# Kernel optimization log

Measured on AMD Instinct MI355X. Metric: run time of the kernel, lower is better.

The kernel has to match this reference:

```python
import jax, jax.numpy as jnp
import numpy as np

LSTM_SIZE = 512
MEM_SIZE = 2048
MEM_DIM = 256
NB_READS = 4
GAMMA = 0.95
EPS = 1e-8
B = 64
IN_RAW = 256
IN_TOTAL = IN_RAW + NB_READS * MEM_SIZE  # 8448
PARAM_DIM = (2 * MEM_DIM + 1) * NB_READS  # 2052


def setup_inputs() -> dict:
    key = jax.random.key(0)
    ks = jax.random.split(key, 8)
    s = 0.02
    return {
        "x": jax.random.normal(ks[0], (B, IN_RAW), jnp.float32),
        "M": jax.random.normal(ks[1], (B, MEM_SIZE, MEM_DIM), jnp.float32),
        "wu": jax.random.uniform(ks[2], (B, MEM_SIZE), jnp.float32),
        "wr": jax.random.uniform(ks[3], (B, NB_READS * MEM_SIZE), jnp.float32),
        "h0": jnp.zeros((LSTM_SIZE,), jnp.float32),
        "c0": jnp.zeros((LSTM_SIZE,), jnp.float32),
        "W_ih": jax.random.normal(ks[4], (4 * LSTM_SIZE, IN_TOTAL), jnp.float32) * s,
        "W_hh": jax.random.normal(ks[5], (4 * LSTM_SIZE, LSTM_SIZE), jnp.float32) * s,
        "b_ih": jnp.zeros((4 * LSTM_SIZE,), jnp.float32),
        "b_hh": jnp.zeros((4 * LSTM_SIZE,), jnp.float32),
        "W_p": jax.random.normal(ks[6], (PARAM_DIM, LSTM_SIZE), jnp.float32) * s,
        "b_p": jax.random.uniform(ks[7], (PARAM_DIM,), jnp.float32, -0.1, 0.1),
    }


def _lstm_scan(x_seq, h0, c0, W_ih, W_hh, b):
    # torch treats the 2-D input as an unbatched sequence of length B:
    # the recurrence runs across the batch axis with a single shared state.
    xW = x_seq @ W_ih.T + b  # [B, 4H] precomputed input contribution

    def step(carry, xw):
        h, c = carry
        g = xw + h @ W_hh.T
        i, f, gg, o = jnp.split(g, 4)
        c = jax.nn.sigmoid(f) * c + jax.nn.sigmoid(i) * jnp.tanh(gg)
        h = jax.nn.sigmoid(o) * jnp.tanh(c)
        return (h, c), h

    (hf, cf), hs = jax.lax.scan(step, (h0, c0), xW)
    return hs, hf, cf


def reference(x, M, wu, wr, h0, c0, W_ih, W_hh, b_ih, b_hh, W_p, b_p):
    ctrl_in = jnp.concatenate([x, wr], axis=-1)  # [B, IN_TOTAL]
    hs, hf, cf = _lstm_scan(ctrl_in, h0, c0, W_ih, W_hh, b_ih + b_hh)
    param = hs @ W_p.T + b_p  # [B, PARAM_DIM]

    nd = NB_READS * MEM_DIM
    k = jnp.tanh(param[:, :nd]).reshape(B, NB_READS, MEM_DIM)
    a = jnp.tanh(param[:, nd:2 * nd]).reshape(B, NB_READS, MEM_DIM)
    sig_alpha = jax.nn.sigmoid(param[:, -NB_READS:])  # [B, R]

    # least_used: topk(wu, k=MEM_SIZE) == full descending sort of indices
    order = jnp.argsort(-wu, axis=-1)  # [B, MEM_SIZE]
    lu_idx = order[:, -1]  # least used slot
    wlu = jax.nn.one_hot(order[:, -NB_READS:], MEM_SIZE, dtype=M.dtype).sum(1)  # [B, N]

    # read head addressing: cosine similarity softmax
    ip = jnp.einsum('brd,bnd->brn', k, M)  # [B, R, N]
    k_norm = jnp.sqrt(jnp.sum(k * k, -1))[:, :, None]
    M_norm = jnp.sqrt(jnp.sum(M * M, -1))[:, None, :]
    wr_t = jax.nn.softmax(ip / (k_norm * M_norm + EPS), axis=-1)  # [B, R, N]

    # write head addressing
    wr_prev3 = wr.reshape(B, NB_READS, MEM_SIZE)
    sa = sig_alpha[:, :, None]
    ww_t = sa * wr_prev3 + (1.0 - sa) * wlu[:, None, :]  # [B, R, N]

    wu_t = GAMMA * wu + wr_t.sum(1) + ww_t.sum(1)  # [B, N]

    erase = 1.0 - jax.nn.one_hot(lu_idx, MEM_SIZE, dtype=M.dtype)  # [B, N]
    M_t = M * erase[:, :, None] + jnp.einsum('brn,brd->bnd', ww_t, a)  # [B, N, D]
    r_t = jnp.einsum('brn,bnd->brd', wr_t, M_t).reshape(B, nd)  # [B, R*D]

    return jnp.concatenate([hs, r_t], axis=-1)  # [B, LSTM+R*D]
```

## Files before the change

kernel.cpp:

```cpp
#include <hip/hip_runtime.h>
#include <hip/hip_bf16.h>

#define BB 64
#define IN_RAW_ 256
#define KIN_ 8448
#define WRW 8192
#define PD_ 2052
#define XW_KS 11
#define XW_CH 768

__global__ __launch_bounds__(256) void k_xw_partial(
    const float* __restrict__ x, const float* __restrict__ wr,
    const float* __restrict__ Wih, float* __restrict__ xwp) {
  const int jb = blockIdx.x & 31;
  const int ks = blockIdx.x >> 5;
  const int j0 = jb << 6;
  const int k0 = ks * XW_CH;
  __shared__ __align__(16) float As[32][68];
  __shared__ __align__(16) float Bs[32][68];
  const int tid = threadIdx.x;
  const int ti = tid & 15, tj = tid >> 4;
  const int lt = tid >> 2, lq = tid & 3;
  float acc[4][4];
#pragma unroll
  for (int i = 0; i < 4; ++i)
#pragma unroll
    for (int j = 0; j < 4; ++j) acc[i][j] = 0.f;
  for (int kc = 0; kc < XW_CH; kc += 32) {
    __syncthreads();
    const int kb = k0 + kc + (lq << 3);
    float va[8], vb[8];
    if (kb < IN_RAW_) {
      const float* p = x + lt * IN_RAW_ + kb;
#pragma unroll
      for (int u = 0; u < 8; ++u) va[u] = p[u];
    } else {
      const float* p = wr + (size_t)lt * WRW + (kb - IN_RAW_);
#pragma unroll
      for (int u = 0; u < 8; ++u) va[u] = p[u];
    }
    {
      const float* p = Wih + (size_t)(j0 + lt) * KIN_ + kb;
#pragma unroll
      for (int u = 0; u < 8; ++u) vb[u] = p[u];
    }
#pragma unroll
    for (int u = 0; u < 8; ++u) As[(lq << 3) + u][lt] = va[u];
#pragma unroll
    for (int u = 0; u < 8; ++u) Bs[(lq << 3) + u][lt] = vb[u];
    __syncthreads();
#pragma unroll
    for (int kk = 0; kk < 32; ++kk) {
      const float4 a4 = *(const float4*)&As[kk][ti << 2];
      const float4 b4 = *(const float4*)&Bs[kk][tj << 2];
      const float av[4] = {a4.x, a4.y, a4.z, a4.w};
      const float bv[4] = {b4.x, b4.y, b4.z, b4.w};
#pragma unroll
      for (int i = 0; i < 4; ++i)
#pragma unroll
        for (int j = 0; j < 4; ++j) acc[i][j] = fmaf(av[i], bv[j], acc[i][j]);
    }
  }
#pragma unroll
  for (int i = 0; i < 4; ++i) {
    const int t = (ti << 2) + i;
    float* dst = xwp + ((size_t)(ks * BB + t) << 11) + j0 + (tj << 2);
    dst[0] = acc[i][0]; dst[1] = acc[i][1]; dst[2] = acc[i][2]; dst[3] = acc[i][3];
  }
}

__global__ __launch_bounds__(64, 1) void k_scan(
    const float* __restrict__ xwp, const float* __restrict__ bih,
    const float* __restrict__ bhh, const float* __restrict__ Whh,
    const float* __restrict__ h0, const float* __restrict__ c0,
    unsigned long long* __restrict__ ht, unsigned long long* __restrict__ xwt,
    float* __restrict__ out, const float* __restrict__ wu,
    int* __restrict__ t4) {
  const int W = blockIdx.x;
  const int l = threadIdx.x;
  if (W >= 192) {
    const int t = W - 192;
    for (int i = 0; i < 32; ++i) {
      const int col = (i << 6) + l;
      float s = bih[col] + bhh[col];
#pragma unroll
      for (int ks = 0; ks < XW_KS; ++ks)
        s += xwp[(size_t)ks * 131072 + (t << 11) + col];
      const unsigned long long pk =
          (1ull << 32) | (unsigned long long)__float_as_uint(s);
      __hip_atomic_store(xwt + (t << 11) + col, pk, __ATOMIC_RELAXED,
                         __HIP_MEMORY_SCOPE_AGENT);
    }
    return;
  }
  if (W >= 128) {
    const int b = W - 128;
    float val[32];
#pragma unroll
    for (int i = 0; i < 32; ++i) val[i] = wu[(b << 11) + (i << 6) + l];
    for (int pick = 0; pick < 4; ++pick) {
      float bv = 3.4e38f; int bi = -1;
// ... 1 lines not shown
      for (int i = 0; i < 32; ++i) {
        const int n = (i << 6) + l;
        const float v = val[i];
        if (v < bv || (v == bv && n > bi)) { bv = v; bi = n; }
      }
#pragma unroll
      for (int s = 1; s < 64; s <<= 1) {
        const float ov = __shfl_xor(bv, s);
        const int oi = __shfl_xor(bi, s);
        if (ov < bv || (ov == bv && oi > bi)) { bv = ov; bi = oi; }
      }
      if (l == 0) t4[(b << 2) + pick] = bi;
      if ((bi & 63) == l) val[bi >> 6] = 3.4e38f;
    }
    return;
  }
  const int d = l & 3;
  const int jj = (W << 2) + d;
  float wreg[16][8];
#pragma unroll
  for (int r = 0; r < 16; ++r) {
    const int row = ((r >> 2) << 9) + (W << 2) + (r & 3);
    const float* p = Whh + ((size_t)row << 9) + (l << 3);
#pragma unroll
    for (int u = 0; u < 8; ++u) wreg[r][u] = p[u];
  }
  float c = 0.f;
  if (l < 4) c = c0[jj];
  float h[8];
#pragma unroll
  for (int u = 0; u < 8; ++u) h[u] = h0[(l << 3) + u];

  for (int t = 0; t < 64; ++t) {
    float xv0 = 0, xv1 = 0, xv2 = 0, xv3 = 0;
    if (l < 4) {
      const unsigned long long* xp = xwt + (t << 11) + jj;
      unsigned long long x0, x1, x2, x3;
      for (;;) {
        x0 = __hip_atomic_load(xp, __ATOMIC_RELAXED, __HIP_MEMORY_SCOPE_AGENT);
        x1 = __hip_atomic_load(xp + 512, __ATOMIC_RELAXED, __HIP_MEMORY_SCOPE_AGENT);
        x2 = __hip_atomic_load(xp + 1024, __ATOMIC_RELAXED, __HIP_MEMORY_SCOPE_AGENT);
        x3 = __hip_atomic_load(xp + 1536, __ATOMIC_RELAXED, __HIP_MEMORY_SCOPE_AGENT);
        if ((unsigned)((x0 & x1 & x2 & x3) >> 32) == 1u) break;
      }
      xv0 = __uint_as_float((unsigned)x0);
      xv1 = __uint_as_float((unsigned)x1);
      xv2 = __uint_as_float((unsigned)x2);
      xv3 = __uint_as_float((unsigned)x3);
    }
    if (t > 0) {
      const unsigned long long* hp = ht + (t << 9) + (l << 3);
      unsigned long long va[8], vb[8];
#pragma unroll
      for (int u = 0; u < 8; ++u)
        va[u] = __hip_atomic_load(hp + u, __ATOMIC_RELAXED, __HIP_MEMORY_SCOPE_AGENT);
      for (;;) {
#pragma unroll
        for (int u = 0; u < 8; ++u)
          vb[u] = __hip_atomic_load(hp + u, __ATOMIC_RELAXED, __HIP_MEMORY_SCOPE_AGENT);
        bool ra = true;
#pragma unroll
        for (int u = 0; u < 8; ++u) ra &= ((unsigned)(va[u] >> 32) == (unsigned)t);
        if (ra) break;
#pragma unroll
        for (int u = 0; u < 8; ++u)
          va[u] = __hip_atomic_load(hp + u, __ATOMIC_RELAXED, __HIP_MEMORY_SCOPE_AGENT);
        bool rb_ = true;
#pragma unroll
        for (int u = 0; u < 8; ++u) rb_ &= ((unsigned)(vb[u] >> 32) == (unsigned)t);
        if (rb_) {
#pragma unroll
          for (int u = 0; u < 8; ++u) va[u] = vb[u];
          break;
        }
      }
#pragma unroll
      for (int u = 0; u < 8; ++u) h[u] = __uint_as_float((unsigned)va[u]);
    }
    float pr[16];
#pragma unroll
    for (int r = 0; r < 16; ++r) {
      float s = 0.f;
#pragma unroll
      for (int u = 0; u < 8; ++u) s = fmaf(wreg[r][u], h[u], s);
      pr[r] = s;
    }
    float v8[8], v4[4], v2[2], v1;
    {
      const bool b0 = (l & 1) != 0;
#pragma unroll
      for (int j = 0; j < 8; ++j) {
        const float keep = b0 ? pr[2 * j + 1] : pr[2 * j];
        const float send = b0 ? pr[2 * j] : pr[2 * j + 1];
        v8[j] = keep + __shfl_xor(send, 1);
      }
    }
    {
      const bool b1 = (l & 2) != 0;
#pragma unroll
      for (int j = 0; j < 4; ++j) {
        const float keep = b1 ? v8[2 * j + 1] : v8[2 * j];
        const float send = b1 ? v8[2 * j] : v8[2 * j + 1];
        v4[j] = keep + __shfl_xor(send, 2);
      }
    }
    {
      const bool b2 = (l & 4) != 0;
#pragma unroll
      for (int j = 0; j < 2; ++j) {
        const float keep = b2 ? v4[2 * j + 1] : v4[2 * j];
// ... 71 lines not shown
#pragma unroll
    for (int u = 0; u < 8; ++u) As[(lq << 3) + u][lt] = va[u];
#pragma unroll
    for (int u = 0; u < 8; ++u) Bs[(lq << 3) + u][lt] = vb[u];
    __syncthreads();
#pragma unroll
    for (int kk = 0; kk < 32; ++kk) {
      const float4 a4 = *(const float4*)&As[kk][ti << 2];
      const float4 b4 = *(const float4*)&Bs[kk][tj << 2];
      const float av[4] = {a4.x, a4.y, a4.z, a4.w};
      const float bv[4] = {b4.x, b4.y, b4.z, b4.w};
#pragma unroll
      for (int i = 0; i < 4; ++i)
#pragma unroll
        for (int j = 0; j < 4; ++j) acc[i][j] = fmaf(av[i], bv[j], acc[i][j]);
    }
  }
#pragma unroll
  for (int i = 0; i < 4; ++i) {
    const int b = (ti << 2) + i;
#pragma unroll
    for (int j = 0; j < 4; ++j) {
      const int col = j0 + (tj << 2) + j;
      if (col < PD_) {
        const float v = acc[i][j] + bp[col];
        if (col < 1024) km[(b << 10) + col] = tanhf(v);
        else if (col < 2048) am[(b << 10) + col - 1024] = tanhf(v);
        else sa[(b << 2) + col - 2048] = 1.f / (1.f + expf(-v));
      }
    }
  }
}

__global__ __launch_bounds__(256) void k_ip(
    const float* __restrict__ M, const float* __restrict__ km,
    float* __restrict__ ip, float* __restrict__ mn) {
  const int b = blockIdx.x >> 4;
  const int nb = blockIdx.x & 15;
  const int n0 = nb << 7;
  const int tid = threadIdx.x;
  const int wv = tid >> 6, l = tid & 63;
  const int q = l >> 4, l16 = l & 15;
  float kr[4][16];
#pragma unroll
  for (int r = 0; r < 4; ++r)
#pragma unroll
    for (int cc = 0; cc < 4; ++cc) {
      const float4 kv = *(const float4*)(km + (((b << 2) + r) << 8) + (cc << 6) + (l16 << 2));
      kr[r][(cc << 2) + 0] = kv.x; kr[r][(cc << 2) + 1] = kv.y;
      kr[r][(cc << 2) + 2] = kv.z; kr[r][(cc << 2) + 3] = kv.w;
    }
  for (int it = 0; it < 8; ++it) {
    const int n = n0 + (wv << 5) + (it << 2) + q;
    const float* mrow = M + (((size_t)b << 11) + n) * 256;
    float s[4] = {0.f, 0.f, 0.f, 0.f};
    float sm = 0.f;
#pragma unroll
    for (int cc = 0; cc < 4; ++cc) {
      const float4 m4 = *(const float4*)(mrow + (cc << 6) + (l16 << 2));
      const float mv[4] = {m4.x, m4.y, m4.z, m4.w};
#pragma unroll
      for (int e = 0; e < 4; ++e) {
        sm = fmaf(mv[e], mv[e], sm);
#pragma unroll
        for (int r = 0; r < 4; ++r) s[r] = fmaf(kr[r][(cc << 2) + e], mv[e], s[r]);
      }
    }
#pragma unroll
    for (int r = 0; r < 4; ++r) {
      float v = s[r];
      v += __shfl_xor(v, 1); v += __shfl_xor(v, 2); v += __shfl_xor(v, 4); v += __shfl_xor(v, 8);
      s[r] = v;
    }
    sm += __shfl_xor(sm, 1); sm += __shfl_xor(sm, 2); sm += __shfl_xor(sm, 4); sm += __shfl_xor(sm, 8);
    if (l16 == 0) {
      const size_t base = ((size_t)b) << 13;
      ip[base + n] = s[0];
      ip[base + 2048 + n] = s[1];
      ip[base + 4096 + n] = s[2];
      ip[base + 6144 + n] = s[3];
      mn[(b << 11) + n] = sqrtf(sm);
    }
  }
}

__global__ __launch_bounds__(512) void k_smrt(
    const float* __restrict__ ip, const float* __restrict__ mn_g,
    const float* __restrict__ sa_g, const float* __restrict__ wr_in,
    const int* __restrict__ t4, const float* __restrict__ am,
    const float* __restrict__ M, const float* __restrict__ km,
    float* __restrict__ out) {
  const int b = blockIdx.x;
  const int tid = threadIdx.x;
  const int wv = tid >> 6, l = tid & 63;
  __shared__ float lam[4][2048];
  __shared__ float mnl[2048];
  __shared__ float Sd[16];
  __shared__ float t4s[4];
  __shared__ float Sl[16];
  __shared__ float wlu4[4];
#pragma unroll
  for (int i = 0; i < 4; ++i) mnl[tid + (i << 9)] = mn_g[(b << 11) + tid + (i << 9)];
  __syncthreads();
  if (wv < 4) {
    const int r = wv;
    const float* kp = km + (b << 10) + (r << 8);
    float sq = 0.f;
#pragma unroll
    for (int i = 0; i < 4; ++i) { const float v = kp[l + (i << 6)]; sq = fmaf(v, v, sq); }
    sq += __shfl_xor(sq, 1);  sq += __shfl_xor(sq, 2);  sq += __shfl_xor(sq, 4);
    sq += __shfl_xor(sq, 8);  sq += __shfl_xor(sq, 16); sq += __shfl_xor(sq, 32);
    const float kn = sqrtf(sq);
    const float* ipr = ip + (((size_t)b) << 13) + ((size_t)r << 11);
    float mx = -3.4e38f;
#pragma unroll 4
    for (int i = 0; i < 32; ++i) {
      const int n = l + (i << 6);
      const float v = ipr[n] / fmaf(kn, mnl[n], 1e-8f);
      lam[r][n] = v;
      mx = fmaxf(mx, v);
    }
    mx = fmaxf(mx, __shfl_xor(mx, 1));  mx = fmaxf(mx, __shfl_xor(mx, 2));
    mx = fmaxf(mx, __shfl_xor(mx, 4));  mx = fmaxf(mx, __shfl_xor(mx, 8));
    mx = fmaxf(mx, __shfl_xor(mx, 16)); mx = fmaxf(mx, __shfl_xor(mx, 32));
    float sum = 0.f;
#pragma unroll 4
    for (int i = 0; i < 32; ++i) {
      const int n = l + (i << 6);
      const float e = expf(lam[r][n] - mx);
      lam[r][n] = e;
      sum += e;
    }
    sum += __shfl_xor(sum, 1);  sum += __shfl_xor(sum, 2);  sum += __shfl_xor(sum, 4);
    sum += __shfl_xor(sum, 8);  sum += __shfl_xor(sum, 16); sum += __shfl_xor(sum, 32);
    const float inv = 1.f / sum;
#pragma unroll 4
    for (int i = 0; i < 32; ++i) {
      const int n = l + (i << 6);
      lam[r][n] *= inv;
    }
  }
  __syncthreads();
#pragma unroll
  for (int j = 0; j < 2; ++j) {
    const int pr = (wv << 1) + j;
    const int r = pr >> 2, qq = pr & 3;
    const float* wp = wr_in + (size_t)b * WRW + (qq << 11);
    float s = 0.f;
#pragma unroll 4
    for (int i = 0; i < 32; ++i) {
      const int n = l + (i << 6);
      s = fmaf(lam[r][n], wp[n], s);
    }
    s += __shfl_xor(s, 1);  s += __shfl_xor(s, 2);  s += __shfl_xor(s, 4);
    s += __shfl_xor(s, 8);  s += __shfl_xor(s, 16); s += __shfl_xor(s, 32);
    if (l == 0) Sd[pr] = s;
  }
  if (tid < 4) {
    float s = 0.f;
#pragma unroll
    for (int ii = 0; ii < 4; ++ii) s += lam[tid][t4[(b << 2) + ii]];
    t4s[tid] = s;
    wlu4[tid] = lam[tid][t4[b << 2]];
  }
  __syncthreads();
  if (tid < 16) {
    const int r = tid >> 2, qq = tid & 3;
    const float sv = sa_g[(b << 2) + qq];
    Sl[tid] = sv * Sd[tid] + (1.f - sv) * t4s[r];
  }
  __syncthreads();
  float4 acc[4];
#pragma unroll
  for (int r = 0; r < 4; ++r) acc[r] = make_float4(0.f, 0.f, 0.f, 0.f);
  const float* Mb = M + (((size_t)b << 11)) * 256;
#pragma unroll 4
  for (int it = 0; it < 256; ++it) {
    const int n = (wv << 8) + it;
    const float4 m4 = *(const float4*)(Mb + (size_t)n * 256 + (l << 2));
#pragma unroll
    for (int r = 0; r < 4; ++r) {
      const float w_ = lam[r][n];
      acc[r].x = fmaf(w_, m4.x, acc[r].x);
      acc[r].y = fmaf(w_, m4.y, acc[r].y);
      acc[r].z = fmaf(w_, m4.z, acc[r].z);
      acc[r].w = fmaf(w_, m4.w, acc[r].w);
    }
  }
  __syncthreads();
  float* red = &lam[0][0];
#pragma unroll
  for (int r = 0; r < 4; ++r)
    *(float4*)(red + (((wv << 2) + r) << 8) + (l << 2)) = acc[r];
  __syncthreads();
  const int luv = t4[b << 2];
#pragma unroll
  for (int i = 0; i < 2; ++i) {
    const int e = tid + (i << 9);
    const int r = e >> 8, d = e & 255;
    float s = -wlu4[r] * M[(((size_t)b << 11) + luv) * 256 + d];
#pragma unroll
    for (int qq = 0; qq < 4; ++qq)
      s = fmaf(Sl[(r << 2) + qq], am[(((b << 2) + qq) << 8) + d], s);
#pragma unroll
    for (int w2 = 0; w2 < 8; ++w2)
      s += red[(((w2 << 2) + r) << 8) + d];
    out[b * 1536 + 512 + e] = s;
  }
}

extern "C" void kernel_launch(void* const* d_in, const int* in_sizes, int n_in,
                              void* d_out, int out_size, void* d_ws, size_t ws_size,
                              hipStream_t stream) {
  (void)in_sizes; (void)n_in; (void)out_size;
  const float* x   = (const float*)d_in[0];
  const float* M   = (const float*)d_in[1];
  const float* wu  = (const float*)d_in[2];
  const float* wr  = (const float*)d_in[3];
  const float* h0  = (const float*)d_in[4];
  const float* c0  = (const float*)d_in[5];
  const float* Wih = (const float*)d_in[6];
  const float* Whh = (const float*)d_in[7];
  const float* bih = (const float*)d_in[8];
  const float* bhh = (const float*)d_in[9];
  const float* Wp  = (const float*)d_in[10];
  const float* bp  = (const float*)d_in[11];
  float* out = (float*)d_out;
  char* ws = (char*)d_ws;
  if (ws_size < 10229760u) return;

  float* xwp = (float*)(ws + 0);
  float* km  = (float*)(ws + 5767168);
  float* am  = (float*)(ws + 6029312);
  float* sa  = (float*)(ws + 6291456);
  int*   t4  = (int*)(ws + 6292480);
  float* ipb = (float*)(ws + 6293504);
  float* mnb = (float*)(ws + 8390656);
  unsigned long long* ht  = (unsigned long long*)(ws + 8914944);
  unsigned long long* xwt = (unsigned long long*)(ws + 9181184);

  hipMemsetAsync(ws + 8914944, 0, 266240 + 1048576, stream);
  hipLaunchKernelGGL(k_xw_partial, dim3(352), dim3(256), 0, stream, x, wr, Wih, xwp);
  hipLaunchKernelGGL(k_scan, dim3(256), dim3(64), 0, stream,
                     xwp, bih, bhh, Whh, h0, c0, ht, xwt, out, wu, t4);
  hipLaunchKernelGGL(k_param, dim3(33), dim3(256), 0, stream, out, Wp, bp, km, am, sa);
  hipLaunchKernelGGL(k_ip, dim3(1024), dim3(256), 0, stream, M, km, ipb, mnb);
  hipLaunchKernelGGL(k_smrt, dim3(64), dim3(512), 0, stream,
                     ipb, mnb, sa, wr, t4, am, M, km, out);
}
```

Measured before the change: 274.0 us.

## Replace tiled input GEMM with transposed-ctrl streaming kernel and reorder scan polling

The shared-memory tiled GEMM for the LSTM input projection is replaced by two kernels. The first transposes the concatenated controller input into a [K,64] layout. The second has each wave compute 8 output columns for all 64 timesteps, reading W_ih directly with per-lane coalesced activation loads and no LDS. In the scan kernel, the xW loads are issued before waiting on h, and the h-poll checks two sentinel words before fetching the remaining six. This trades an extra launch and transpose pass for more parallel blocks and lower-latency polling; the W_ih reads are now scalar and uncoalesced across lanes, which may hurt bandwidth.

```diff
diff --git a/kernel.cpp b/kernel.cpp
--- a/kernel.cpp
+++ b/kernel.cpp
@@ -7,66 +7,62 @@
 #define WRW 8192
 #define PD_ 2052
 #define XW_KS 11
-#define XW_CH 768
-
-__global__ __launch_bounds__(256) void k_xw_partial(
+
+__global__ __launch_bounds__(256) void k_ctrlT(
     const float* __restrict__ x, const float* __restrict__ wr,
-    const float* __restrict__ Wih, float* __restrict__ xwp) {
-  const int jb = blockIdx.x & 31;
-  const int ks = blockIdx.x >> 5;
-  const int j0 = jb << 6;
-  const int k0 = ks * XW_CH;
-  __shared__ __align__(16) float As[32][68];
-  __shared__ __align__(16) float Bs[32][68];
+    float* __restrict__ ctrlT) {
+  const int kb = blockIdx.x << 5;
   const int tid = threadIdx.x;
-  const int ti = tid & 15, tj = tid >> 4;
-  const int lt = tid >> 2, lq = tid & 3;
-  float acc[4][4];
-#pragma unroll
-  for (int i = 0; i < 4; ++i)
-#pragma unroll
-    for (int j = 0; j < 4; ++j) acc[i][j] = 0.f;
-  for (int kc = 0; kc < XW_CH; kc += 32) {
-    __syncthreads();
-    const int kb = k0 + kc + (lq << 3);
-    float va[8], vb[8];
-    if (kb < IN_RAW_) {
-      const float* p = x + lt * IN_RAW_ + kb;
-#pragma unroll
-      for (int u = 0; u < 8; ++u) va[u] = p[u];
-    } else {
-      const float* p = wr + (size_t)lt * WRW + (kb - IN_RAW_);
-#pragma unroll
-      for (int u = 0; u < 8; ++u) va[u] = p[u];
-    }
-    {
-      const float* p = Wih + (size_t)(j0 + lt) * KIN_ + kb;
-#pragma unroll
-      for (int u = 0; u < 8; ++u) vb[u] = p[u];
-    }
-#pragma unroll
-    for (int u = 0; u < 8; ++u) As[(lq << 3) + u][lt] = va[u];
-#pragma unroll
-    for (int u = 0; u < 8; ++u) Bs[(lq << 3) + u][lt] = vb[u];
-    __syncthreads();
-#pragma unroll
-    for (int kk = 0; kk < 32; ++kk) {
-      const float4 a4 = *(const float4*)&As[kk][ti << 2];
-      const float4 b4 = *(const float4*)&Bs[kk][tj << 2];
-      const float av[4] = {a4.x, a4.y, a4.z, a4.w};
-      const float bv[4] = {b4.x, b4.y, b4.z, b4.w};
-#pragma unroll
-      for (int i = 0; i < 4; ++i)
-#pragma unroll
-        for (int j = 0; j < 4; ++j) acc[i][j] = fmaf(av[i], bv[j], acc[i][j]);
-    }
-  }
-#pragma unroll
-  for (int i = 0; i < 4; ++i) {
-    const int t = (ti << 2) + i;
-    float* dst = xwp + ((size_t)(ks * BB + t) << 11) + j0 + (tj << 2);
-    dst[0] = acc[i][0]; dst[1] = acc[i][1]; dst[2] = acc[i][2]; dst[3] = acc[i][3];
-  }
+  __shared__ float ld[32][65];
+#pragma unroll
+  for (int pass = 0; pass < 8; ++pass) {
+    const int t = (tid >> 5) + (pass << 3);
+    const int k = tid & 31;
+    const int kk = kb + k;
+    const float v = (kk < IN_RAW_) ? x[t * IN_RAW_ + kk]
+                                   : wr[(size_t)t * WRW + kk - IN_RAW_];
+    ld[k][t] = v;
+  }
+  __syncthreads();
+#pragma unroll
+  for (int pass = 0; pass < 8; ++pass) {
+    const int k = (tid >> 6) + (pass << 2);
+    ctrlT[(size_t)(kb + k) * 64 + (tid & 63)] = ld[k][tid & 63];
+  }
+}
+
+__global__ __launch_bounds__(256) void k_xw2(
+    const float* __restrict__ ctrlT, const float* __restrict__ Wih,
+    float* __restrict__ xwp) {
+  const int cb = blockIdx.x & 63;
+  const int ks = blockIdx.x >> 6;
+  const int k0 = ks * 768;
+  const int wv = __builtin_amdgcn_readfirstlane(threadIdx.x >> 6);
+  const int l = threadIdx.x & 63;
+  const int c0 = (cb << 5) + (wv << 3);
+  const float* at = ctrlT + (size_t)k0 * 64 + l;
+  const float* wb = Wih + (size_t)c0 * KIN_ + k0;
+  float acc[8];
+#pragma unroll
+  for (int c = 0; c < 8; ++c) acc[c] = 0.f;
+#pragma unroll 2
+  for (int k = 0; k < 768; k += 4) {
+    const float a0 = at[(size_t)(k + 0) << 6];
+    const float a1 = at[(size_t)(k + 1) << 6];
+    const float a2 = at[(size_t)(k + 2) << 6];
+    const float a3 = at[(size_t)(k + 3) << 6];
+#pragma unroll
+    for (int c = 0; c < 8; ++c) {
+      const float* wp = wb + (size_t)c * KIN_ + k;
+      acc[c] = fmaf(a0, wp[0], acc[c]);
+      acc[c] = fmaf(a1, wp[1], acc[c]);
+      acc[c] = fmaf(a2, wp[2], acc[c]);
+      acc[c] = fmaf(a3, wp[3], acc[c]);
+    }
+  }
+  float* dst = xwp + (size_t)ks * 131072 + (l << 11) + c0;
+  *(float4*)(dst) = make_float4(acc[0], acc[1], acc[2], acc[3]);
+  *(float4*)(dst + 4) = make_float4(acc[4], acc[5], acc[6], acc[7]);
 }
 
 __global__ __launch_bounds__(64, 1) void k_scan(
@@ -134,50 +130,57 @@
   for (int u = 0; u < 8; ++u) h[u] = h0[(l << 3) + u];
 
   for (int t = 0; t < 64; ++t) {
+    const unsigned long long* xp = xwt + (t << 11) + jj;
+    unsigned long long x0 = 0, x1 = 0, x2 = 0, x3 = 0;
+    if (l < 4) {
+      x0 = __hip_atomic_load(xp, __ATOMIC_RELAXED, __HIP_MEMORY_SCOPE_AGENT);
+      x1 = __hip_atomic_load(xp + 512, __ATOMIC_RELAXED, __HIP_MEMORY_SCOPE_AGENT);
+      x2 = __hip_atomic_load(xp + 1024, __ATOMIC_RELAXED, __HIP_MEMORY_SCOPE_AGENT);
+      x3 = __hip_atomic_load(xp + 1536, __ATOMIC_RELAXED, __HIP_MEMORY_SCOPE_AGENT);
+    }
+    if (t > 0) {
+      const unsigned long long* hp = ht + (t << 9) + (l << 3);
+      unsigned long long v[8];
+      for (;;) {
+        const unsigned long long s0 =
+            __hip_atomic_load(hp, __ATOMIC_RELAXED, __HIP_MEMORY_SCOPE_AGENT);
+        const unsigned long long s4 =
+            __hip_atomic_load(hp + 4, __ATOMIC_RELAXED, __HIP_MEMORY_SCOPE_AGENT);
+        if (((unsigned)(s0 >> 32) == (unsigned)t) &&
+            ((unsigned)(s4 >> 32) == (unsigned)t)) {
+          v[0] = s0; v[4] = s4;
+          v[1] = __hip_atomic_load(hp + 1, __ATOMIC_RELAXED, __HIP_MEMORY_SCOPE_AGENT);
+          v[2] = __hip_atomic_load(hp + 2, __ATOMIC_RELAXED, __HIP_MEMORY_SCOPE_AGENT);
+          v[3] = __hip_atomic_load(hp + 3, __ATOMIC_RELAXED, __HIP_MEMORY_SCOPE_AGENT);
+          v[5] = __hip_atomic_load(hp + 5, __ATOMIC_RELAXED, __HIP_MEMORY_SCOPE_AGENT);
+          v[6] = __hip_atomic_load(hp + 6, __ATOMIC_RELAXED, __HIP_MEMORY_SCOPE_AGENT);
+          v[7] = __hip_atomic_load(hp + 7, __ATOMIC_RELAXED, __HIP_MEMORY_SCOPE_AGENT);
+          bool ok = true;
+          ok &= ((unsigned)(v[1] >> 32) == (unsigned)t);
+          ok &= ((unsigned)(v[2] >> 32) == (unsigned)t);
+          ok &= ((unsigned)(v[3] >> 32) == (unsigned)t);
+          ok &= ((unsigned)(v[5] >> 32) == (unsigned)t);
+          ok &= ((unsigned)(v[6] >> 32) == (unsigned)t);
+          ok &= ((unsigned)(v[7] >> 32) == (unsigned)t);
+          if (ok) break;
+        }
+      }
+#pragma unroll
+      for (int u = 0; u < 8; ++u) h[u] = __uint_as_float((unsigned)v[u]);
+    }
     float xv0 = 0, xv1 = 0, xv2 = 0, xv3 = 0;
     if (l < 4) {
-      const unsigned long long* xp = xwt + (t << 11) + jj;
-      unsigned long long x0, x1, x2, x3;
-      for (;;) {
+      while (!(((unsigned)(x0 >> 32) == 1u) && ((unsigned)(x1 >> 32) == 1u) &&
+               ((unsigned)(x2 >> 32) == 1u) && ((unsigned)(x3 >> 32) == 1u))) {
         x0 = __hip_atomic_load(xp, __ATOMIC_RELAXED, __HIP_MEMORY_SCOPE_AGENT);
         x1 = __hip_atomic_load(xp + 512, __ATOMIC_RELAXED, __HIP_MEMORY_SCOPE_AGENT);
         x2 = __hip_atomic_load(xp + 1024, __ATOMIC_RELAXED, __HIP_MEMORY_SCOPE_AGENT);
         x3 = __hip_atomic_load(xp + 1536, __ATOMIC_RELAXED, __HIP_MEMORY_SCOPE_AGENT);
-        if ((unsigned)((x0 & x1 & x2 & x3) >> 32) == 1u) break;
       }
       xv0 = __uint_as_float((unsigned)x0);
       xv1 = __uint_as_float((unsigned)x1);
       xv2 = __uint_as_float((unsigned)x2);
       xv3 = __uint_as_float((unsigned)x3);
-    }
-    if (t > 0) {
-      const unsigned long long* hp = ht + (t << 9) + (l << 3);
-      unsigned long long va[8], vb[8];
-#pragma unroll
-      for (int u = 0; u < 8; ++u)
-        va[u] = __hip_atomic_load(hp + u, __ATOMIC_RELAXED, __HIP_MEMORY_SCOPE_AGENT);
-      for (;;) {
-#pragma unroll
-        for (int u = 0; u < 8; ++u)
-          vb[u] = __hip_atomic_load(hp + u, __ATOMIC_RELAXED, __HIP_MEMORY_SCOPE_AGENT);
-        bool ra = true;
-#pragma unroll
-        for (int u = 0; u < 8; ++u) ra &= ((unsigned)(va[u] >> 32) == (unsigned)t);
-        if (ra) break;
-#pragma unroll
-        for (int u = 0; u < 8; ++u)
-          va[u] = __hip_atomic_load(hp + u, __ATOMIC_RELAXED, __HIP_MEMORY_SCOPE_AGENT);
-        bool rb_ = true;
-#pragma unroll
-        for (int u = 0; u < 8; ++u) rb_ &= ((unsigned)(vb[u] >> 32) == (unsigned)t);
-        if (rb_) {
-#pragma unroll
-          for (int u = 0; u < 8; ++u) va[u] = vb[u];
-          break;
-        }
-      }
-#pragma unroll
-      for (int u = 0; u < 8; ++u) h[u] = __uint_as_float((unsigned)va[u]);
     }
     float pr[16];
 #pragma unroll
@@ -510,7 +513,7 @@
   const float* bp  = (const float*)d_in[11];
   float* out = (float*)d_out;
   char* ws = (char*)d_ws;
-  if (ws_size < 10229760u) return;
+  if (ws_size < 12392448u) return;
 
   float* xwp = (float*)(ws + 0);
   float* km  = (float*)(ws + 5767168);
@@ -521,9 +524,11 @@
   float* mnb = (float*)(ws + 8390656);
   unsigned long long* ht  = (unsigned long long*)(ws + 8914944);
   unsigned long long* xwt = (unsigned long long*)(ws + 9181184);
+  float* ctrlT = (float*)(ws + 10229760);
 
   hipMemsetAsync(ws + 8914944, 0, 266240 + 1048576, stream);
-  hipLaunchKernelGGL(k_xw_partial, dim3(352), dim3(256), 0, stream, x, wr, Wih, xwp);
+  hipLaunchKernelGGL(k_ctrlT, dim3(264), dim3(256), 0, stream, x, wr, ctrlT);
+  hipLaunchKernelGGL(k_xw2, dim3(704), dim3(256), 0, stream, ctrlT, Wih, xwp);
   hipLaunchKernelGGL(k_scan, dim3(256), dim3(64), 0, stream,
                      xwp, bih, bhh, Whh, h0, c0, ht, xwt, out, wu, t4);
   hipLaunchKernelGGL(k_param, dim3(33), dim3(256), 0, stream, out, Wp, bp, km, am, sa);
```

After: 405.7 us. +48.0%, slower.

## Widen xW GEMM tiles to 64x128 with 16 K-splits and streamline scan polling

Applied to the files above, without the earlier changes.

The input-projection GEMM now uses 128-column tiles with 4x8 register accumulators and 16 K-slices of 544 (the last is 288), launching 256 blocks instead of 352. Each block reuses its A tile across twice as many columns and writes results as float4. The scan's spin-wait is restructured: xW loads are issued before the h wait, and h polling checks two sentinel words before loading the rest. The partial-sum buffer grows, which shifts workspace offsets, and the scan's reduction over K-slices must match the new XW_KS of 16.

```diff
diff --git a/kernel.cpp b/kernel.cpp
--- a/kernel.cpp
+++ b/kernel.cpp
@@ -6,30 +6,30 @@
 #define KIN_ 8448
 #define WRW 8192
 #define PD_ 2052
-#define XW_KS 11
-#define XW_CH 768
+#define XW_KS 16
 
 __global__ __launch_bounds__(256) void k_xw_partial(
     const float* __restrict__ x, const float* __restrict__ wr,
     const float* __restrict__ Wih, float* __restrict__ xwp) {
-  const int jb = blockIdx.x & 31;
-  const int ks = blockIdx.x >> 5;
-  const int j0 = jb << 6;
-  const int k0 = ks * XW_CH;
+  const int cb = blockIdx.x & 15;
+  const int ks = blockIdx.x >> 4;
+  const int j0 = cb << 7;
+  const int k0 = ks * 544;
+  const int klen = (ks == 15) ? 288 : 544;
   __shared__ __align__(16) float As[32][68];
-  __shared__ __align__(16) float Bs[32][68];
+  __shared__ __align__(16) float Bs[32][136];
   const int tid = threadIdx.x;
   const int ti = tid & 15, tj = tid >> 4;
   const int lt = tid >> 2, lq = tid & 3;
-  float acc[4][4];
+  float acc[4][8];
 #pragma unroll
   for (int i = 0; i < 4; ++i)
 #pragma unroll
-    for (int j = 0; j < 4; ++j) acc[i][j] = 0.f;
-  for (int kc = 0; kc < XW_CH; kc += 32) {
+    for (int j = 0; j < 8; ++j) acc[i][j] = 0.f;
+  for (int kc = 0; kc < klen; kc += 32) {
     __syncthreads();
     const int kb = k0 + kc + (lq << 3);
-    float va[8], vb[8];
+    float va[8], vb0[8], vb1[8];
     if (kb < IN_RAW_) {
       const float* p = x + lt * IN_RAW_ + kb;
 #pragma unroll
@@ -42,30 +42,38 @@
     {
       const float* p = Wih + (size_t)(j0 + lt) * KIN_ + kb;
 #pragma unroll
-      for (int u = 0; u < 8; ++u) vb[u] = p[u];
+      for (int u = 0; u < 8; ++u) vb0[u] = p[u];
+      const float* p2 = Wih + (size_t)(j0 + 64 + lt) * KIN_ + kb;
+#pragma unroll
+      for (int u = 0; u < 8; ++u) vb1[u] = p2[u];
     }
 #pragma unroll
     for (int u = 0; u < 8; ++u) As[(lq << 3) + u][lt] = va[u];
 #pragma unroll
-    for (int u = 0; u < 8; ++u) Bs[(lq << 3) + u][lt] = vb[u];
+    for (int u = 0; u < 8; ++u) Bs[(lq << 3) + u][lt] = vb0[u];
+#pragma unroll
+    for (int u = 0; u < 8; ++u) Bs[(lq << 3) + u][64 + lt] = vb1[u];
     __syncthreads();
 #pragma unroll
     for (int kk = 0; kk < 32; ++kk) {
       const float4 a4 = *(const float4*)&As[kk][ti << 2];
-      const float4 b4 = *(const float4*)&Bs[kk][tj << 2];
+      const float4 b4a = *(const float4*)&Bs[kk][tj << 3];
+      const float4 b4b = *(const float4*)&Bs[kk][(tj << 3) + 4];
       const float av[4] = {a4.x, a4.y, a4.z, a4.w};
-      const float bv[4] = {b4.x, b4.y, b4.z, b4.w};
+      const float bv[8] = {b4a.x, b4a.y, b4a.z, b4a.w,
+                           b4b.x, b4b.y, b4b.z, b4b.w};
 #pragma unroll
       for (int i = 0; i < 4; ++i)
 #pragma unroll
-        for (int j = 0; j < 4; ++j) acc[i][j] = fmaf(av[i], bv[j], acc[i][j]);
+        for (int j = 0; j < 8; ++j) acc[i][j] = fmaf(av[i], bv[j], acc[i][j]);
     }
   }
 #pragma unroll
   for (int i = 0; i < 4; ++i) {
     const int t = (ti << 2) + i;
-    float* dst = xwp + ((size_t)(ks * BB + t) << 11) + j0 + (tj << 2);
-    dst[0] = acc[i][0]; dst[1] = acc[i][1]; dst[2] = acc[i][2]; dst[3] = acc[i][3];
+    float* dst = xwp + (size_t)ks * 131072 + (t << 11) + j0 + (tj << 3);
+    *(float4*)(dst) = make_float4(acc[i][0], acc[i][1], acc[i][2], acc[i][3]);
+    *(float4*)(dst + 4) = make_float4(acc[i][4], acc[i][5], acc[i][6], acc[i][7]);
   }
 }
 
@@ -134,50 +142,57 @@
   for (int u = 0; u < 8; ++u) h[u] = h0[(l << 3) + u];
 
   for (int t = 0; t < 64; ++t) {
+    const unsigned long long* xp = xwt + (t << 11) + jj;
+    unsigned long long x0 = 0, x1 = 0, x2 = 0, x3 = 0;
+    if (l < 4) {
+      x0 = __hip_atomic_load(xp, __ATOMIC_RELAXED, __HIP_MEMORY_SCOPE_AGENT);
+      x1 = __hip_atomic_load(xp + 512, __ATOMIC_RELAXED, __HIP_MEMORY_SCOPE_AGENT);
+      x2 = __hip_atomic_load(xp + 1024, __ATOMIC_RELAXED, __HIP_MEMORY_SCOPE_AGENT);
+      x3 = __hip_atomic_load(xp + 1536, __ATOMIC_RELAXED, __HIP_MEMORY_SCOPE_AGENT);
+    }
+    if (t > 0) {
+      const unsigned long long* hp = ht + (t << 9) + (l << 3);
+      unsigned long long v[8];
+      for (;;) {
+        const unsigned long long s0 =
+            __hip_atomic_load(hp, __ATOMIC_RELAXED, __HIP_MEMORY_SCOPE_AGENT);
+        const unsigned long long s4 =
+            __hip_atomic_load(hp + 4, __ATOMIC_RELAXED, __HIP_MEMORY_SCOPE_AGENT);
+        if (((unsigned)(s0 >> 32) == (unsigned)t) &&
+            ((unsigned)(s4 >> 32) == (unsigned)t)) {
+          v[0] = s0; v[4] = s4;
+          v[1] = __hip_atomic_load(hp + 1, __ATOMIC_RELAXED, __HIP_MEMORY_SCOPE_AGENT);
+          v[2] = __hip_atomic_load(hp + 2, __ATOMIC_RELAXED, __HIP_MEMORY_SCOPE_AGENT);
+          v[3] = __hip_atomic_load(hp + 3, __ATOMIC_RELAXED, __HIP_MEMORY_SCOPE_AGENT);
+          v[5] = __hip_atomic_load(hp + 5, __ATOMIC_RELAXED, __HIP_MEMORY_SCOPE_AGENT);
+          v[6] = __hip_atomic_load(hp + 6, __ATOMIC_RELAXED, __HIP_MEMORY_SCOPE_AGENT);
+          v[7] = __hip_atomic_load(hp + 7, __ATOMIC_RELAXED, __HIP_MEMORY_SCOPE_AGENT);
+          bool ok = true;
+          ok &= ((unsigned)(v[1] >> 32) == (unsigned)t);
+          ok &= ((unsigned)(v[2] >> 32) == (unsigned)t);
+          ok &= ((unsigned)(v[3] >> 32) == (unsigned)t);
+          ok &= ((unsigned)(v[5] >> 32) == (unsigned)t);
+          ok &= ((unsigned)(v[6] >> 32) == (unsigned)t);
+          ok &= ((unsigned)(v[7] >> 32) == (unsigned)t);
+          if (ok) break;
+        }
+      }
+#pragma unroll
+      for (int u = 0; u < 8; ++u) h[u] = __uint_as_float((unsigned)v[u]);
+    }
     float xv0 = 0, xv1 = 0, xv2 = 0, xv3 = 0;
     if (l < 4) {
-      const unsigned long long* xp = xwt + (t << 11) + jj;
-      unsigned long long x0, x1, x2, x3;
-      for (;;) {
+      while (!(((unsigned)(x0 >> 32) == 1u) && ((unsigned)(x1 >> 32) == 1u) &&
+               ((unsigned)(x2 >> 32) == 1u) && ((unsigned)(x3 >> 32) == 1u))) {
         x0 = __hip_atomic_load(xp, __ATOMIC_RELAXED, __HIP_MEMORY_SCOPE_AGENT);
         x1 = __hip_atomic_load(xp + 512, __ATOMIC_RELAXED, __HIP_MEMORY_SCOPE_AGENT);
         x2 = __hip_atomic_load(xp + 1024, __ATOMIC_RELAXED, __HIP_MEMORY_SCOPE_AGENT);
         x3 = __hip_atomic_load(xp + 1536, __ATOMIC_RELAXED, __HIP_MEMORY_SCOPE_AGENT);
-        if ((unsigned)((x0 & x1 & x2 & x3) >> 32) == 1u) break;
       }
       xv0 = __uint_as_float((unsigned)x0);
       xv1 = __uint_as_float((unsigned)x1);
       xv2 = __uint_as_float((unsigned)x2);
       xv3 = __uint_as_float((unsigned)x3);
-    }
-    if (t > 0) {
-      const unsigned long long* hp = ht + (t << 9) + (l << 3);
-      unsigned long long va[8], vb[8];
-#pragma unroll
-      for (int u = 0; u < 8; ++u)
-        va[u] = __hip_atomic_load(hp + u, __ATOMIC_RELAXED, __HIP_MEMORY_SCOPE_AGENT);
-      for (;;) {
-#pragma unroll
-        for (int u = 0; u < 8; ++u)
-          vb[u] = __hip_atomic_load(hp + u, __ATOMIC_RELAXED, __HIP_MEMORY_SCOPE_AGENT);
-        bool ra = true;
-#pragma unroll
-        for (int u = 0; u < 8; ++u) ra &= ((unsigned)(va[u] >> 32) == (unsigned)t);
-        if (ra) break;
-#pragma unroll
-        for (int u = 0; u < 8; ++u)
-          va[u] = __hip_atomic_load(hp + u, __ATOMIC_RELAXED, __HIP_MEMORY_SCOPE_AGENT);
-        bool rb_ = true;
-#pragma unroll
-        for (int u = 0; u < 8; ++u) rb_ &= ((unsigned)(vb[u] >> 32) == (unsigned)t);
-        if (rb_) {
-#pragma unroll
-          for (int u = 0; u < 8; ++u) va[u] = vb[u];
-          break;
-        }
-      }
-#pragma unroll
-      for (int u = 0; u < 8; ++u) h[u] = __uint_as_float((unsigned)va[u]);
     }
     float pr[16];
 #pragma unroll
@@ -510,20 +525,20 @@
   const float* bp  = (const float*)d_in[11];
   float* out = (float*)d_out;
   char* ws = (char*)d_ws;
-  if (ws_size < 10229760u) return;
+  if (ws_size < 12851200u) return;
 
   float* xwp = (float*)(ws + 0);
-  float* km  = (float*)(ws + 5767168);
-  float* am  = (float*)(ws + 6029312);
-  float* sa  = (float*)(ws + 6291456);
-  int*   t4  = (int*)(ws + 6292480);
-  float* ipb = (float*)(ws + 6293504);
-  float* mnb = (float*)(ws + 8390656);
-  unsigned long long* ht  = (unsigned long long*)(ws + 8914944);
-  unsigned long long* xwt = (unsigned long long*)(ws + 9181184);
-
-  hipMemsetAsync(ws + 8914944, 0, 266240 + 1048576, stream);
-  hipLaunchKernelGGL(k_xw_partial, dim3(352), dim3(256), 0, stream, x, wr, Wih, xwp);
+  float* km  = (float*)(ws + 8388608);
+  float* am  = (float*)(ws + 8650752);
+  float* sa  = (float*)(ws + 8912896);
+  int*   t4  = (int*)(ws + 8913920);
+  float* ipb = (float*)(ws + 8914944);
+  float* mnb = (float*)(ws + 11012096);
+  unsigned long long* ht  = (unsigned long long*)(ws + 11536384);
+  unsigned long long* xwt = (unsigned long long*)(ws + 11802624);
+
+  hipMemsetAsync(ws + 11536384, 0, 266240 + 1048576, stream);
+  hipLaunchKernelGGL(k_xw_partial, dim3(256), dim3(256), 0, stream, x, wr, Wih, xwp);
   hipLaunchKernelGGL(k_scan, dim3(256), dim3(64), 0, stream,
                      xwp, bih, bhh, Whh, h0, c0, ht, xwt, out, wu, t4);
   hipLaunchKernelGGL(k_param, dim3(33), dim3(256), 0, stream, out, Wp, bp, km, am, sa);
```

New measurement: 314.1 us. +14.6%, slower.

## Fuse similarity, softmax and memory read into one pass over M

Applied to the files above, without the earlier changes.

Replaces the separate inner-product kernel and the per-batch softmax/read kernel with a split kernel. It computes cosine similarities, unnormalized exponentials (no max subtraction, since cosine values are bounded) and the weighted memory read in a single pass over M per slice, then writes partial sums. A small finalize kernel sums the 8 slices per batch and applies normalization and the write-head terms. This removes the second full read of M and spreads the read across 512 blocks instead of 64, at the cost of more registers per thread and extra partial-buffer traffic.

```diff
diff --git a/kernel.cpp b/kernel.cpp
--- a/kernel.cpp
+++ b/kernel.cpp
@@ -315,179 +315,197 @@
   }
 }
 
-__global__ __launch_bounds__(256) void k_ip(
+__global__ __launch_bounds__(256) void k_ipv(
     const float* __restrict__ M, const float* __restrict__ km,
-    float* __restrict__ ip, float* __restrict__ mn) {
-  const int b = blockIdx.x >> 4;
-  const int nb = blockIdx.x & 15;
-  const int n0 = nb << 7;
+    const float* __restrict__ wr_in, const int* __restrict__ t4,
+    float* __restrict__ pacc, float* __restrict__ pscal) {
+  const int b = blockIdx.x >> 3;
+  const int sl = blockIdx.x & 7;
   const int tid = threadIdx.x;
   const int wv = tid >> 6, l = tid & 63;
-  const int q = l >> 4, l16 = l & 15;
+  const int g = l >> 4, j = l & 15;
+  __shared__ float kns[4];
+  __shared__ float t4eL[4][4];
+  __shared__ __align__(16) float accW[4][4][256];
+  __shared__ float SdW[4][4][4];
+  __shared__ float ssW[4][4];
+  if (tid < 16) t4eL[tid >> 2][tid & 3] = 0.f;
+  {
+    const float* kp = km + (((b << 2) + wv) << 8);
+    float sq = 0.f;
+#pragma unroll
+    for (int i = 0; i < 4; ++i) { const float v = kp[l + (i << 6)]; sq = fmaf(v, v, sq); }
+    sq += __shfl_xor(sq, 1);  sq += __shfl_xor(sq, 2);  sq += __shfl_xor(sq, 4);
+    sq += __shfl_xor(sq, 8);  sq += __shfl_xor(sq, 16); sq += __shfl_xor(sq, 32);
+    if (l == 0) kns[wv] = sqrtf(sq);
+  }
   float kr[4][16];
 #pragma unroll
   for (int r = 0; r < 4; ++r)
 #pragma unroll
     for (int cc = 0; cc < 4; ++cc) {
-      const float4 kv = *(const float4*)(km + (((b << 2) + r) << 8) + (cc << 6) + (l16 << 2));
+      const float4 kv = *(const float4*)(km + (((b << 2) + r) << 8) + (cc << 6) + (j << 2));
       kr[r][(cc << 2) + 0] = kv.x; kr[r][(cc << 2) + 1] = kv.y;
       kr[r][(cc << 2) + 2] = kv.z; kr[r][(cc << 2) + 3] = kv.w;
     }
-  for (int it = 0; it < 8; ++it) {
-    const int n = n0 + (wv << 5) + (it << 2) + q;
+  int t4v[4];
+#pragma unroll
+  for (int ii = 0; ii < 4; ++ii) t4v[ii] = t4[(b << 2) + ii];
+  __syncthreads();
+  const float kn0 = kns[0], kn1 = kns[1], kn2 = kns[2], kn3 = kns[3];
+  float aacc[4][16];
+#pragma unroll
+  for (int r = 0; r < 4; ++r)
+#pragma unroll
+    for (int k = 0; k < 16; ++k) aacc[r][k] = 0.f;
+  float ssum[4] = {0.f, 0.f, 0.f, 0.f};
+  float sdp[4] = {0.f, 0.f, 0.f, 0.f};
+  for (int it = 0; it < 16; ++it) {
+    const int n = (sl << 8) + (wv << 6) + (it << 2) + g;
     const float* mrow = M + (((size_t)b << 11) + n) * 256;
-    float s[4] = {0.f, 0.f, 0.f, 0.f};
-    float sm = 0.f;
+    float4 m4[4];
+#pragma unroll
+    for (int cc = 0; cc < 4; ++cc)
+      m4[cc] = *(const float4*)(mrow + (cc << 6) + (j << 2));
+    float s0 = 0.f, s1 = 0.f, s2 = 0.f, s3 = 0.f, sm = 0.f;
 #pragma unroll
     for (int cc = 0; cc < 4; ++cc) {
-      const float4 m4 = *(const float4*)(mrow + (cc << 6) + (l16 << 2));
-      const float mv[4] = {m4.x, m4.y, m4.z, m4.w};
+      const float mv[4] = {m4[cc].x, m4[cc].y, m4[cc].z, m4[cc].w};
 #pragma unroll
       for (int e = 0; e < 4; ++e) {
         sm = fmaf(mv[e], mv[e], sm);
-#pragma unroll
-        for (int r = 0; r < 4; ++r) s[r] = fmaf(kr[r][(cc << 2) + e], mv[e], s[r]);
-      }
-    }
+        s0 = fmaf(kr[0][(cc << 2) + e], mv[e], s0);
+        s1 = fmaf(kr[1][(cc << 2) + e], mv[e], s1);
+        s2 = fmaf(kr[2][(cc << 2) + e], mv[e], s2);
+        s3 = fmaf(kr[3][(cc << 2) + e], mv[e], s3);
+      }
+    }
+    s0 += __shfl_xor(s0, 1); s0 += __shfl_xor(s0, 2); s0 += __shfl_xor(s0, 4); s0 += __shfl_xor(s0, 8);
+    s1 += __shfl_xor(s1, 1); s1 += __shfl_xor(s1, 2); s1 += __shfl_xor(s1, 4); s1 += __shfl_xor(s1, 8);
+    s2 += __shfl_xor(s2, 1); s2 += __shfl_xor(s2, 2); s2 += __shfl_xor(s2, 4); s2 += __shfl_xor(s2, 8);
+    s3 += __shfl_xor(s3, 1); s3 += __shfl_xor(s3, 2); s3 += __shfl_xor(s3, 4); s3 += __shfl_xor(s3, 8);
+    sm += __shfl_xor(sm, 1); sm += __shfl_xor(sm, 2); sm += __shfl_xor(sm, 4); sm += __shfl_xor(sm, 8);
+    const float mnv = sqrtf(sm);
+    float ev[4];
+    ev[0] = __expf(s0 / fmaf(kn0, mnv, 1e-8f));
+    ev[1] = __expf(s1 / fmaf(kn1, mnv, 1e-8f));
+    ev[2] = __expf(s2 / fmaf(kn2, mnv, 1e-8f));
+    ev[3] = __expf(s3 / fmaf(kn3, mnv, 1e-8f));
 #pragma unroll
     for (int r = 0; r < 4; ++r) {
-      float v = s[r];
-      v += __shfl_xor(v, 1); v += __shfl_xor(v, 2); v += __shfl_xor(v, 4); v += __shfl_xor(v, 8);
-      s[r] = v;
-    }
-    sm += __shfl_xor(sm, 1); sm += __shfl_xor(sm, 2); sm += __shfl_xor(sm, 4); sm += __shfl_xor(sm, 8);
-    if (l16 == 0) {
-      const size_t base = ((size_t)b) << 13;
-      ip[base + n] = s[0];
-      ip[base + 2048 + n] = s[1];
-      ip[base + 4096 + n] = s[2];
-      ip[base + 6144 + n] = s[3];
-      mn[(b << 11) + n] = sqrtf(sm);
-    }
+      ssum[r] += ev[r];
+#pragma unroll
+      for (int cc = 0; cc < 4; ++cc) {
+        aacc[r][(cc << 2) + 0] = fmaf(ev[r], m4[cc].x, aacc[r][(cc << 2) + 0]);
+        aacc[r][(cc << 2) + 1] = fmaf(ev[r], m4[cc].y, aacc[r][(cc << 2) + 1]);
+        aacc[r][(cc << 2) + 2] = fmaf(ev[r], m4[cc].z, aacc[r][(cc << 2) + 2]);
+        aacc[r][(cc << 2) + 3] = fmaf(ev[r], m4[cc].w, aacc[r][(cc << 2) + 3]);
+      }
+    }
+    if (j < 4) {
+      const float wq = wr_in[((size_t)b << 13) + (j << 11) + n];
+#pragma unroll
+      for (int r = 0; r < 4; ++r) sdp[r] = fmaf(ev[r], wq, sdp[r]);
+    }
+#pragma unroll
+    for (int ii = 0; ii < 4; ++ii)
+      if (n == t4v[ii] && j == 0) {
+#pragma unroll
+        for (int r = 0; r < 4; ++r) t4eL[ii][r] = ev[r];
+      }
+  }
+#pragma unroll
+  for (int r = 0; r < 4; ++r) {
+    float v = ssum[r];
+    v += __shfl_xor(v, 1);  v += __shfl_xor(v, 2);  v += __shfl_xor(v, 4);
+    v += __shfl_xor(v, 8);  v += __shfl_xor(v, 16); v += __shfl_xor(v, 32);
+    if (l == 0) ssW[wv][r] = v * 0.0625f;
+    float sdv = sdp[r];
+    sdv += __shfl_xor(sdv, 16);
+    sdv += __shfl_xor(sdv, 32);
+    if (l < 4) SdW[wv][l][r] = sdv;
+  }
+#pragma unroll
+  for (int r = 0; r < 4; ++r)
+#pragma unroll
+    for (int k = 0; k < 16; ++k) {
+      float v = aacc[r][k];
+      v += __shfl_xor(v, 16);
+      v += __shfl_xor(v, 32);
+      aacc[r][k] = v;
+    }
+  if (l < 16) {
+#pragma unroll
+    for (int r = 0; r < 4; ++r)
+#pragma unroll
+      for (int cc = 0; cc < 4; ++cc)
+#pragma unroll
+        for (int ee = 0; ee < 4; ++ee)
+          accW[wv][r][(cc << 6) + (l << 2) + ee] = aacc[r][(cc << 2) + ee];
+  }
+  __syncthreads();
+  const int slice = (b << 3) + sl;
+#pragma unroll
+  for (int i = 0; i < 4; ++i) {
+    const int e = tid + (i << 8);
+    const float s4 = accW[0][i][tid] + accW[1][i][tid] + accW[2][i][tid] + accW[3][i][tid];
+    pacc[((size_t)slice << 10) + e] = s4;
+  }
+  if (tid < 4)
+    pscal[(slice << 6) + tid] = ssW[0][tid] + ssW[1][tid] + ssW[2][tid] + ssW[3][tid];
+  if (tid < 16) {
+    const int r = tid >> 2, q = tid & 3;
+    pscal[(slice << 6) + 4 + (r << 2) + q] =
+        SdW[0][q][r] + SdW[1][q][r] + SdW[2][q][r] + SdW[3][q][r];
+    pscal[(slice << 6) + 20 + tid] = t4eL[tid >> 2][tid & 3];
   }
 }
 
-__global__ __launch_bounds__(512) void k_smrt(
-    const float* __restrict__ ip, const float* __restrict__ mn_g,
-    const float* __restrict__ sa_g, const float* __restrict__ wr_in,
-    const int* __restrict__ t4, const float* __restrict__ am,
-    const float* __restrict__ M, const float* __restrict__ km,
+__global__ __launch_bounds__(256) void k_fin(
+    const float* __restrict__ pacc, const float* __restrict__ pscal,
+    const float* __restrict__ sa_g, const float* __restrict__ am,
+    const float* __restrict__ M, const int* __restrict__ t4,
     float* __restrict__ out) {
   const int b = blockIdx.x;
   const int tid = threadIdx.x;
-  const int wv = tid >> 6, l = tid & 63;
-  __shared__ float lam[4][2048];
-  __shared__ float mnl[2048];
-  __shared__ float Sd[16];
-  __shared__ float t4s[4];
-  __shared__ float Sl[16];
-  __shared__ float wlu4[4];
-#pragma unroll
-  for (int i = 0; i < 4; ++i) mnl[tid + (i << 9)] = mn_g[(b << 11) + tid + (i << 9)];
-  __syncthreads();
-  if (wv < 4) {
-    const int r = wv;
-    const float* kp = km + (b << 10) + (r << 8);
-    float sq = 0.f;
-#pragma unroll
-    for (int i = 0; i < 4; ++i) { const float v = kp[l + (i << 6)]; sq = fmaf(v, v, sq); }
-    sq += __shfl_xor(sq, 1);  sq += __shfl_xor(sq, 2);  sq += __shfl_xor(sq, 4);
-    sq += __shfl_xor(sq, 8);  sq += __shfl_xor(sq, 16); sq += __shfl_xor(sq, 32);
-    const float kn = sqrtf(sq);
-    const float* ipr = ip + (((size_t)b) << 13) + ((size_t)r << 11);
-    float mx = -3.4e38f;
-#pragma unroll 4
-    for (int i = 0; i < 32; ++i) {
-      const int n = l + (i << 6);
-      const float v = ipr[n] / fmaf(kn, mnl[n], 1e-8f);
-      lam[r][n] = v;
-      mx = fmaxf(mx, v);
-    }
-    mx = fmaxf(mx, __shfl_xor(mx, 1));  mx = fmaxf(mx, __shfl_xor(mx, 2));
-    mx = fmaxf(mx, __shfl_xor(mx, 4));  mx = fmaxf(mx, __shfl_xor(mx, 8));
-    mx = fmaxf(mx, __shfl_xor(mx, 16)); mx = fmaxf(mx, __shfl_xor(mx, 32));
-    float sum = 0.f;
-#pragma unroll 4
-    for (int i = 0; i < 32; ++i) {
-      const int n = l + (i << 6);
-      const float e = expf(lam[r][n] - mx);
-      lam[r][n] = e;
-      sum += e;
-    }
-    sum += __shfl_xor(sum, 1);  sum += __shfl_xor(sum, 2);  sum += __shfl_xor(sum, 4);
-    sum += __shfl_xor(sum, 8);  sum += __shfl_xor(sum, 16); sum += __shfl_xor(sum, 32);
-    const float inv = 1.f / sum;
-#pragma unroll 4
-    for (int i = 0; i < 32; ++i) {
-      const int n = l + (i << 6);
-      lam[r][n] *= inv;
-    }
-  }
-  __syncthreads();
-#pragma unroll
-  for (int j = 0; j < 2; ++j) {
-    const int pr = (wv << 1) + j;
-    const int r = pr >> 2, qq = pr & 3;
-    const float* wp = wr_in + (size_t)b * WRW + (qq << 11);
-    float s = 0.f;
-#pragma unroll 4
-    for (int i = 0; i < 32; ++i) {
-      const int n = l + (i << 6);
-      s = fmaf(lam[r][n], wp[n], s);
-    }
-    s += __shfl_xor(s, 1);  s += __shfl_xor(s, 2);  s += __shfl_xor(s, 4);
-    s += __shfl_xor(s, 8);  s += __shfl_xor(s, 16); s += __shfl_xor(s, 32);
-    if (l == 0) Sd[pr] = s;
-  }
+  __shared__ float Zs[4], Sl[16], wlu4[4], teL[4][4];
   if (tid < 4) {
-    float s = 0.f;
-#pragma unroll
-    for (int ii = 0; ii < 4; ++ii) s += lam[tid][t4[(b << 2) + ii]];
-    t4s[tid] = s;
-    wlu4[tid] = lam[tid][t4[b << 2]];
+    float z = 0.f;
+    for (int sl = 0; sl < 8; ++sl) z += pscal[(((b << 3) + sl) << 6) + tid];
+    Zs[tid] = z;
+  }
+  if (tid >= 16 && tid < 32) {
+    const int ii = (tid - 16) >> 2, r = (tid - 16) & 3;
+    float te = 0.f;
+    for (int sl = 0; sl < 8; ++sl)
+      te += pscal[(((b << 3) + sl) << 6) + 20 + (ii << 2) + r];
+    teL[ii][r] = te;
   }
   __syncthreads();
   if (tid < 16) {
-    const int r = tid >> 2, qq = tid & 3;
-    const float sv = sa_g[(b << 2) + qq];
-    Sl[tid] = sv * Sd[tid] + (1.f - sv) * t4s[r];
-  }
-  __syncthreads();
-  float4 acc[4];
-#pragma unroll
-  for (int r = 0; r < 4; ++r) acc[r] = make_float4(0.f, 0.f, 0.f, 0.f);
-  const float* Mb = M + (((size_t)b << 11)) * 256;
-#pragma unroll 4
-  for (int it = 0; it < 256; ++it) {
-    const int n = (wv << 8) + it;
-    const float4 m4 = *(const float4*)(Mb + (size_t)n * 256 + (l << 2));
-#pragma unroll
-    for (int r = 0; r < 4; ++r) {
-      const float w_ = lam[r][n];
-      acc[r].x = fmaf(w_, m4.x, acc[r].x);
-      acc[r].y = fmaf(w_, m4.y, acc[r].y);
-      acc[r].z = fmaf(w_, m4.z, acc[r].z);
-      acc[r].w = fmaf(w_, m4.w, acc[r].w);
-    }
-  }
-  __syncthreads();
-  float* red = &lam[0][0];
-#pragma unroll
-  for (int r = 0; r < 4; ++r)
-    *(float4*)(red + (((wv << 2) + r) << 8) + (l << 2)) = acc[r];
+    const int r = tid >> 2, q = tid & 3;
+    float sd = 0.f;
+    for (int sl = 0; sl < 8; ++sl)
+      sd += pscal[(((b << 3) + sl) << 6) + 4 + (r << 2) + q];
+    const float Z = Zs[r];
+    const float t4s = (teL[0][r] + teL[1][r] + teL[2][r] + teL[3][r]) / Z;
+    const float sv = sa_g[(b << 2) + q];
+    Sl[(r << 2) + q] = sv * (sd / Z) + (1.f - sv) * t4s;
+    if (q == 0) wlu4[r] = teL[0][r] / Z;
+  }
   __syncthreads();
   const int luv = t4[b << 2];
 #pragma unroll
-  for (int i = 0; i < 2; ++i) {
-    const int e = tid + (i << 9);
-    const int r = e >> 8, d = e & 255;
-    float s = -wlu4[r] * M[(((size_t)b << 11) + luv) * 256 + d];
-#pragma unroll
-    for (int qq = 0; qq < 4; ++qq)
-      s = fmaf(Sl[(r << 2) + qq], am[(((b << 2) + qq) << 8) + d], s);
-#pragma unroll
-    for (int w2 = 0; w2 < 8; ++w2)
-      s += red[(((w2 << 2) + r) << 8) + d];
+  for (int i = 0; i < 4; ++i) {
+    const int e = tid + (i << 8);
+    float s = 0.f;
+    for (int sl = 0; sl < 8; ++sl)
+      s += pacc[((size_t)(((b << 3) + sl)) << 10) + e];
+    s /= Zs[i];
+    s -= wlu4[i] * M[(((size_t)b << 11) + luv) * 256 + tid];
+#pragma unroll
+    for (int q = 0; q < 4; ++q)
+      s = fmaf(Sl[(i << 2) + q], am[(((b << 2) + q) << 8) + tid], s);
     out[b * 1536 + 512 + e] = s;
   }
 }
@@ -510,24 +528,24 @@
   const float* bp  = (const float*)d_in[11];
   float* out = (float*)d_out;
   char* ws = (char*)d_ws;
-  if (ws_size < 10229760u) return;
-
-  float* xwp = (float*)(ws + 0);
-  float* km  = (float*)(ws + 5767168);
-  float* am  = (float*)(ws + 6029312);
-  float* sa  = (float*)(ws + 6291456);
-  int*   t4  = (int*)(ws + 6292480);
-  float* ipb = (float*)(ws + 6293504);
-  float* mnb = (float*)(ws + 8390656);
-  unsigned long long* ht  = (unsigned long long*)(ws + 8914944);
-  unsigned long long* xwt = (unsigned long long*)(ws + 9181184);
-
-  hipMemsetAsync(ws + 8914944, 0, 266240 + 1048576, stream);
+  if (ws_size < 9836544u) return;
+
+  float* xwp  = (float*)(ws + 0);
+  float* km   = (float*)(ws + 5767168);
+  float* am   = (float*)(ws + 6029312);
+  float* sa   = (float*)(ws + 6291456);
+  int*   t4   = (int*)(ws + 6292480);
+  float* pacc = (float*)(ws + 6293504);
+  float* pscal= (float*)(ws + 8390656);
+  unsigned long long* ht  = (unsigned long long*)(ws + 8521728);
+  unsigned long long* xwt = (unsigned long long*)(ws + 8787968);
+
+  (void)hipMemsetAsync(ws + 8521728, 0, 266240 + 1048576, stream);
   hipLaunchKernelGGL(k_xw_partial, dim3(352), dim3(256), 0, stream, x, wr, Wih, xwp);
   hipLaunchKernelGGL(k_scan, dim3(256), dim3(64), 0, stream,
                      xwp, bih, bhh, Whh, h0, c0, ht, xwt, out, wu, t4);
   hipLaunchKernelGGL(k_param, dim3(33), dim3(256), 0, stream, out, Wp, bp, km, am, sa);
-  hipLaunchKernelGGL(k_ip, dim3(1024), dim3(256), 0, stream, M, km, ipb, mnb);
-  hipLaunchKernelGGL(k_smrt, dim3(64), dim3(512), 0, stream,
-                     ipb, mnb, sa, wr, t4, am, M, km, out);
+  hipLaunchKernelGGL(k_ipv, dim3(512), dim3(256), 0, stream, M, km, wr, t4, pacc, pscal);
+  hipLaunchKernelGGL(k_fin, dim3(64), dim3(256), 0, stream,
+                     pacc, pscal, sa, am, M, t4, out);
 }
```

Measured after the change: 250.3 us. 8.7% less time.
